# Kernel optimization log

Measured on AMD Instinct MI355X. Metric: run time of the kernel, lower is better.

## Reference

```python
import jax, jax.numpy as jnp
import numpy as np

SEQ_LEN = 1
INPUT = 2048
HIDDEN = 2048
CLASSES = 10
K = int(np.floor(np.sqrt(HIDDEN)))            # avgKernelSize = 45
NUM_EH = (HIDDEN - K) // K + 1                # 45 pooled features
LENGTHS = (32, 128, 512)                      # EHlengths (window sizes)
EST_DIM = NUM_EH * len(LENGTHS) * 2           # mean + variance per (feature, window)
B = 8192


def setup_inputs() -> dict:
    key = jax.random.key(0)
    ks = jax.random.split(key, 7)
    s = 1.0 / np.sqrt(HIDDEN)
    u = lambda k, shape: jax.random.uniform(k, shape, jnp.float32, -s, s)
    return {
        "x": jax.random.normal(ks[0], (B, SEQ_LEN, INPUT), jnp.float32),
        "W_ih": u(ks[1], (HIDDEN, INPUT)),
        "W_hh": u(ks[2], (HIDDEN, HIDDEN)),
        "b_ih": u(ks[3], (HIDDEN,)),
        "b_hh": u(ks[4], (HIDDEN,)),
        "W_lin": u(ks[5], (CLASSES, HIDDEN + EST_DIM)),
        "b_lin": u(ks[6], (CLASSES,)),
    }


def _sliding_stats(pooled):
    """Causal sliding-window mean/variance over the batch/stream axis.

    pooled: (B, F). Returns (B, F, J, 2) with [..., 0]=mean, [..., 1]=var.
    This is the exact quantity the VarEH exponential histograms approximate
    (streaming mean/variance over the last L elements added).
    """
    n = pooled.shape[0]
    cs = jnp.cumsum(pooled, axis=0)
    cs2 = jnp.cumsum(pooled * pooled, axis=0)
    idx = jnp.arange(n)
    outs = []
    for L in LENGTHS:  # small fixed set of window lengths
        zpad = jnp.zeros((L,) + pooled.shape[1:], pooled.dtype)
        cs_l = jnp.concatenate([zpad, cs], axis=0)[:n]
        cs2_l = jnp.concatenate([zpad, cs2], axis=0)[:n]
        cnt = jnp.minimum(idx + 1, L).astype(pooled.dtype)[:, None]
        m = (cs - cs_l) / cnt
        v = (cs2 - cs2_l) / cnt - m * m
        outs.append(jnp.stack([m, v], axis=-1))  # (B, F, 2)
    return jnp.stack(outs, axis=2)  # (B, F, J, 2)


def reference(x, W_ih, W_hh, b_ih, b_hh, W_lin, b_lin):
    b = x.shape[0]
    # Elman RNN, batch_first, h0 = 0. Precompute input projection for all steps.
    xw = jnp.einsum("bsi,hi->bsh", x, W_ih) + b_ih + b_hh  # (B, S, H)

    def step(h, xt):
        h = jnp.tanh(xt + h @ W_hh.T)
        return h, h

    h0 = jnp.zeros((b, HIDDEN), x.dtype)
    _, hs = jax.lax.scan(step, h0, jnp.swapaxes(xw, 0, 1))  # (S, B, H)
    rnn_out = hs[-1]  # (B, H); with seq_len=1 this equals squeeze(rnn_out)

    # AvgPool1d(kernel=K, stride=K) over hidden dim -> (B, NUM_EH)
    pooled = rnn_out[:, : NUM_EH * K].reshape(b, NUM_EH, K).mean(axis=-1)

    # Streaming mean/var estimates across the batch stream (VarEH semantics)
    est = _sliding_stats(pooled).reshape(b, EST_DIM)

    lin_in = jnp.concatenate([rnn_out, est], axis=1)  # (B, H + EST_DIM)
    logits = lin_in @ W_lin.T + b_lin
    return jax.nn.softmax(logits, axis=1)
```

## Files before the change

### kernel.cpp

```cpp
#include <hip/hip_runtime.h>
#include <hip/hip_bf16.h>
#include <math.h>

typedef short s16x8 __attribute__((ext_vector_type(8)));
typedef float f32x4 __attribute__((ext_vector_type(4)));

__device__ inline unsigned short f2bf(float x) {
    unsigned int u = __float_as_uint(x);
    unsigned int r = (u + 0x7fffu + ((u >> 16) & 1u)) >> 16;
    return (unsigned short)r;
}
__device__ inline float bf2f(unsigned short u) {
    return __uint_as_float(((unsigned int)u) << 16);
}

__device__ inline float fast_tanh(float x) {
    float e = __expf(2.0f * x);
    return 1.0f - 2.0f * __builtin_amdgcn_rcpf(e + 1.0f);
}

__global__ void cvtprep_kernel(const float* __restrict__ x,
                               const float* __restrict__ W_ih,
                               const float* __restrict__ W_lin,
                               unsigned short* __restrict__ xb,
                               unsigned short* __restrict__ wb,
                               unsigned short* __restrict__ wlb) {
    int blk = blockIdx.x;
    int tid = threadIdx.x;
    if (blk < 16384) {
        int i = blk * 256 + tid;
        float4 v = ((const float4*)x)[i];
        ushort4 o; o.x = f2bf(v.x); o.y = f2bf(v.y); o.z = f2bf(v.z); o.w = f2bf(v.w);
        ((ushort4*)xb)[i] = o;
    } else if (blk < 20480) {
        int i = (blk - 16384) * 256 + tid;
        float4 v = ((const float4*)W_ih)[i];
        ushort4 o; o.x = f2bf(v.x); o.y = f2bf(v.y); o.z = f2bf(v.z); o.w = f2bf(v.w);
        ((ushort4*)wb)[i] = o;
    } else {
        int idx = (blk - 20480) * 256 + tid;
        if (idx < 37376) {
            int c = idx / 2336, k = idx - c * 2336;
            float v = (c < 10 && k < 2318) ? W_lin[c * 2318 + k] : 0.f;
            wlb[idx] = f2bf(v);
        }
    }
}


#define MFMA_(a, b, c) __builtin_amdgcn_mfma_f32_16x16x32_bf16(a, b, c, 0, 0, 0)

__device__ inline s16x8 frag_ld(const unsigned short* hbase, int row, int ksub, int quad) {
    int slot = (ksub * 4 + quad) ^ (row & 7);
    return *(const s16x8*)(hbase + row * 64 + slot * 8);
}

__device__ inline void stage_u(const unsigned short* __restrict__ gmat, int half,
                               int rowoff, int kt, unsigned short* lmat, int tid) {
    int r = tid >> 3, s = tid & 7;
    int lr = rowoff + r;
    int ks = (s ^ (lr & 7)) << 3;
    const unsigned short* gp = gmat + (size_t)(half * 128 + lr) * 2048 + kt * 64 + ks;
    __builtin_amdgcn_global_load_lds(
        (const __attribute__((address_space(1))) void*)gp,
        (__attribute__((address_space(3))) void*)(lmat + half * 8192 + lr * 64 + s * 8),
        16, 0, 0);
}

#define LOAD_AQ(q)                                                       \
    af0 = frag_ld(Ah, (q) * 32 +      mrow, 0, quad);                    \
    af1 = frag_ld(Ah, (q) * 32 + 16 + mrow, 0, quad);                    \
    af2 = frag_ld(Ah, (q) * 32 +      mrow, 1, quad);                    \
    af3 = frag_ld(Ah, (q) * 32 + 16 + mrow, 1, quad);

#define MFMA_Q(q)                                                        \
    acc[(q)*2 + 0][0] = MFMA_(af0, bf00, acc[(q)*2 + 0][0]);             \
    acc[(q)*2 + 0][1] = MFMA_(af0, bf01, acc[(q)*2 + 0][1]);             \
    acc[(q)*2 + 0][2] = MFMA_(af0, bf02, acc[(q)*2 + 0][2]);             \
    acc[(q)*2 + 0][3] = MFMA_(af0, bf03, acc[(q)*2 + 0][3]);             \
    acc[(q)*2 + 1][0] = MFMA_(af1, bf00, acc[(q)*2 + 1][0]);             \
    acc[(q)*2 + 1][1] = MFMA_(af1, bf01, acc[(q)*2 + 1][1]);             \
    acc[(q)*2 + 1][2] = MFMA_(af1, bf02, acc[(q)*2 + 1][2]);             \
    acc[(q)*2 + 1][3] = MFMA_(af1, bf03, acc[(q)*2 + 1][3]);             \
    acc[(q)*2 + 0][0] = MFMA_(af2, bf10, acc[(q)*2 + 0][0]);             \
    acc[(q)*2 + 0][1] = MFMA_(af2, bf11, acc[(q)*2 + 0][1]);             \
    acc[(q)*2 + 0][2] = MFMA_(af2, bf12, acc[(q)*2 + 0][2]);             \
    acc[(q)*2 + 0][3] = MFMA_(af2, bf13, acc[(q)*2 + 0][3]);             \
    acc[(q)*2 + 1][0] = MFMA_(af3, bf10, acc[(q)*2 + 1][0]);             \
    acc[(q)*2 + 1][1] = MFMA_(af3, bf11, acc[(q)*2 + 1][1]);             \
    acc[(q)*2 + 1][2] = MFMA_(af3, bf12, acc[(q)*2 + 1][2]);             \
    acc[(q)*2 + 1][3] = MFMA_(af3, bf13, acc[(q)*2 + 1][3]);

#define PHASE_CORE(q)                                                    \
    __builtin_amdgcn_s_barrier();                                        \
    asm volatile("s_waitcnt lgkmcnt(0)" ::: "memory");                   \
    __builtin_amdgcn_s_setprio(1);                                       \
    MFMA_Q(q);                                                           \
    __builtin_amdgcn_s_setprio(0);

__global__ __launch_bounds__(512) void gemm_tanh_kernel(
    const unsigned short* __restrict__ A, const unsigned short* __restrict__ Bm,
    const float* __restrict__ b_ih, const float* __restrict__ b_hh,
    unsigned short* __restrict__ Hb)
{
    __shared__ __align__(16) unsigned short lds[2][2][16384];

    const int tid  = threadIdx.x;
    const int lane = tid & 63;
    const int wave = tid >> 6;
    const int wgid = blockIdx.x;
    const int cblk = wgid & 7;
    const int rblk = wgid >> 3;
    const int row0 = rblk * 256;
    const int col0 = cblk * 256;
    const int wm   = wave >> 2;
    const int wn   = wave & 3;
    const int quad = lane >> 4;
    const int mrow = lane & 15;
    const int NT   = 32;

    const unsigned short* Ag = A  + (size_t)row0 * 2048;
    const unsigned short* Bg = Bm + (size_t)col0 * 2048;

    f32x4 acc[8][4];
#pragma unroll
    for (int i = 0; i < 8; ++i)
#pragma unroll
        for (int j = 0; j < 4; ++j) acc[i][j] = f32x4{0.f, 0.f, 0.f, 0.f};

    stage_u(Ag, 0, 0,  0, lds[0][0], tid);  stage_u(Ag, 0, 64, 0, lds[0][0], tid);
    stage_u(Ag, 1, 0,  0, lds[0][0], tid);  stage_u(Ag, 1, 64, 0, lds[0][0], tid);
    stage_u(Bg, 0, 0,  0, lds[0][1], tid);  stage_u(Bg, 0, 64, 0, lds[0][1], tid);
    stage_u(Bg, 1, 0,  0, lds[0][1], tid);  stage_u(Bg, 1, 64, 0, lds[0][1], tid);
    stage_u(Bg, 0, 0,  1, lds[1][1], tid);  stage_u(Bg, 0, 64, 1, lds[1][1], tid);
    stage_u(Bg, 1, 0,  1, lds[1][1], tid);  stage_u(Bg, 1, 64, 1, lds[1][1], tid);
    stage_u(Ag, 0, 0,  1, lds[1][0], tid);  stage_u(Ag, 1, 0,  1, lds[1][0], tid);
    asm volatile("s_waitcnt vmcnt(6)" ::: "memory");
    __builtin_amdgcn_s_barrier();

    for (int t = 0; t < NT; ++t) {
        const int buf = t & 1;
        unsigned short* LA  = lds[buf][0];
        unsigned short* LB  = lds[buf][1];
        unsigned short* NLA = lds[buf ^ 1][0];
        const unsigned short* Ah = LA + wm * 8192;
        const unsigned short* Bh = LB + (wn >> 1) * 8192;
        const int bco = (wn & 1) * 64;

        s16x8 bf00, bf01, bf02, bf03, bf10, bf11, bf12, bf13;
        s16x8 af0, af1, af2, af3;

        bf00 = frag_ld(Bh, bco +  0 + mrow, 0, quad);
        bf01 = frag_ld(Bh, bco + 16 + mrow, 0, quad);
        bf02 = frag_ld(Bh, bco + 32 + mrow, 0, quad);
        bf03 = frag_ld(Bh, bco + 48 + mrow, 0, quad);
        bf10 = frag_ld(Bh, bco +  0 + mrow, 1, quad);
        bf11 = frag_ld(Bh, bco + 16 + mrow, 1, quad);
        bf12 = frag_ld(Bh, bco + 32 + mrow, 1, quad);
        bf13 = frag_ld(Bh, bco + 48 + mrow, 1, quad);
        LOAD_AQ(0);
        if (t + 1 < NT) {
            stage_u(Ag, 0, 64, t + 1, NLA, tid);
            stage_u(Ag, 1, 64, t + 1, NLA, tid);
        }
        asm volatile("s_waitcnt lgkmcnt(8)" ::: "memory");
        PHASE_CORE(0);
        __builtin_amdgcn_s_barrier();

        LOAD_AQ(1);
        if (t + 2 < NT) {
            stage_u(Bg, 0, 0,  t + 2, LB, tid);
            stage_u(Bg, 0, 64, t + 2, LB, tid);
        }
        PHASE_CORE(1);
        __builtin_amdgcn_s_barrier();

        LOAD_AQ(2);
        if (t + 2 < NT) {
            stage_u(Bg, 1, 0,  t + 2, LB, tid);
            stage_u(Bg, 1, 64, t + 2, LB, tid);
        }
        PHASE_CORE(2);
        __builtin_amdgcn_s_barrier();

        LOAD_AQ(3);
        if (t + 2 < NT) {
            stage_u(Ag, 0, 0, t + 2, LA, tid);
            stage_u(Ag, 1, 0, t + 2, LA, tid);
        }
        PHASE_CORE(3);
        if (t + 2 < NT) {
            asm volatile("s_waitcnt vmcnt(6)" ::: "memory");
        } else if (t + 1 < NT) {
            asm volatile("s_waitcnt vmcnt(0)" ::: "memory");
        }
        __builtin_amdgcn_s_barrier();
    }

    float bias[4];
#pragma unroll
    for (int j = 0; j < 4; ++j) {
        int gc = col0 + wn * 64 + j * 16 + mrow;
        bias[j] = b_ih[gc] + b_hh[gc];
    }
#pragma unroll
    for (int i = 0; i < 8; ++i) {
#pragma unroll
        for (int rr = 0; rr < 4; ++rr) {
            int grow = row0 + wm * 128 + i * 16 + quad * 4 + rr;
#pragma unroll
            for (int j = 0; j < 4; ++j) {
                int gc = col0 + wn * 64 + j * 16 + mrow;
                float v = acc[i][j][rr] + bias[j];
                Hb[(size_t)grow * 2048 + gc] = f2bf(fast_tanh(v));
            }
        }
    }
}

__global__ __launch_bounds__(256) void pool_kernel(
    const unsigned short* __restrict__ Hb, float* __restrict__ pooled_t) {
    __shared__ unsigned short hs[8 * 2048];
    __shared__ float outs[45 * 8];
    int b0 = blockIdx.x * 8;
    int tid = threadIdx.x;
    const ushort4* src = (const ushort4*)(Hb + (size_t)b0 * 2048);
    ushort4* dst = (ushort4*)hs;
    for (int i = tid; i < 4096; i += 256) dst[i] = src[i];
    __syncthreads();
    for (int o = tid; o < 360; o += 256) {
        int f = o % 45, r = o / 45;
        const unsigned short* row = hs + r * 2048 + f * 45;
        float s = 0.f;
#pragma unroll
        for (int k = 0; k < 45; ++k) s += bf2f(row[k]);
        outs[f * 8 + r] = s * (1.0f / 45.0f);
    }
    __syncthreads();
    for (int o = tid; o < 360; o += 256) {
        int f = o >> 3, r = o & 7;
        pooled_t[f * 8192 + b0 + r] = outs[o];
    }
}

__global__ __launch_bounds__(256) void scan_kernel(
    const float* __restrict__ pooled_t,
    float* __restrict__ cs_t, float* __restrict__ cs2_t) {
    __shared__ float t1[256], t2[256];
    int f = blockIdx.x;
    int tid = threadIdx.x;
    const float* p = pooled_t + f * 8192;
    int base = tid * 32;
    float loc[32];
    float s1 = 0.f, s2 = 0.f;
#pragma unroll
    for (int i = 0; i < 32; ++i) {
        float v = p[base + i];
        loc[i] = v; s1 += v; s2 += v * v;
    }
    t1[tid] = s1; t2[tid] = s2;
    __syncthreads();
    for (int d = 1; d < 256; d <<= 1) {
        float a1 = (tid >= d) ? t1[tid - d] : 0.f;
        float a2 = (tid >= d) ? t2[tid - d] : 0.f;
        __syncthreads();
        t1[tid] += a1; t2[tid] += a2;
        __syncthreads();
    }
    float r1 = t1[tid] - s1, r2 = t2[tid] - s2;
    float* c1 = cs_t + f * 8192;
    float* c2 = cs2_t + f * 8192;
#pragma unroll
    for (int i = 0; i < 32; ++i) {
        float v = loc[i];
        r1 += v; r2 += v * v;
        c1[base + i] = r1; c2[base + i] = r2;
    }
}

#define ESTRIDE 290
__global__ __launch_bounds__(256) void final_kernel(
    const unsigned short* __restrict__ Hb,
    const float* __restrict__ cs_t, const float* __restrict__ cs2_t,
    const unsigned short* __restrict__ Wb, const float* __restrict__ b_lin,
    float* __restrict__ out) {
    __shared__ unsigned short Es[32 * ESTRIDE];
    __shared__ float comb[2 * 16 * 17];
    int tid = threadIdx.x;
    int lane = tid & 63;
    int wave = tid >> 6;
    int b0 = blockIdx.x * 32;

    for (int i = tid; i < 135 * 32; i += 256) {
        int fj = i >> 5, r = i & 31;
        int f = fj / 3, j = fj - 3 * f;
        int b = b0 + r;
        int L = (j == 0) ? 32 : (j == 1) ? 128 : 512;
        const float* c1 = cs_t + f * 8192;
        const float* c2 = cs2_t + f * 8192;
        float a1 = c1[b], a2 = c2[b];
        float p1 = 0.f, p2 = 0.f;
        if (b >= L) { p1 = c1[b - L]; p2 = c2[b - L]; }
        float cnt = (float)((b + 1 < L) ? (b + 1) : L);
        float m = (a1 - p1) / cnt;
        float v = (a2 - p2) / cnt - m * m;
        int d0 = f * 6 + j * 2;
        Es[r * ESTRIDE + d0]     = f2bf(m);
        Es[r * ESTRIDE + d0 + 1] = f2bf(v);
    }
    for (int i = tid; i < 32 * 18; i += 256) {
        int r = i / 18, d = 270 + i % 18;
        Es[r * ESTRIDE + d] = 0;
    }
    __syncthreads();

    const int t = wave >> 1;
    const int kh = wave & 1;
    const int quad = lane >> 4;
    const int mrow = lane & 15;
    const int rowt = b0 + t * 16;

    f32x4 acc = f32x4{0.f, 0.f, 0.f, 0.f};
    const unsigned short* arow = Hb + (size_t)(rowt + mrow) * 2048 + kh * 1024 + quad * 8;
    const unsigned short* brow = Wb + (size_t)mrow * 2336 + kh * 1024 + quad * 8;
#pragma unroll 4
    for (int k = 0; k < 1024; k += 32) {
        s16x8 a = *(const s16x8*)(arow + k);
        s16x8 b = *(const s16x8*)(brow + k);
        acc = __builtin_amdgcn_mfma_f32_16x16x32_bf16(a, b, acc, 0, 0, 0);
    }
    if (kh) {
        const unsigned short* erow = Es + (t * 16 + mrow) * ESTRIDE + quad * 8;
        const unsigned short* wrow = Wb + (size_t)mrow * 2336 + 2048 + quad * 8;
#pragma unroll
        for (int k = 0; k < 288; k += 32) {
            s16x8 a = *(const s16x8*)(erow + k);
            s16x8 b = *(const s16x8*)(wrow + k);
            acc = __builtin_amdgcn_mfma_f32_16x16x32_bf16(a, b, acc, 0, 0, 0);
        }
    }

    float* cb = comb + t * 272;
    if (kh == 0) {
#pragma unroll
        for (int r = 0; r < 4; ++r) cb[(quad * 4 + r) * 17 + mrow] = acc[r];
    }
    __syncthreads();
    if (kh == 1) {
#pragma unroll
        for (int r = 0; r < 4; ++r) cb[(quad * 4 + r) * 17 + mrow] += acc[r];
    }
    __syncthreads();

    if (tid < 32) {
        const float* base = comb + (tid >> 4) * 272 + (tid & 15) * 17;
        float lg[10];
        float mx = -1e30f;
#pragma unroll
        for (int c = 0; c < 10; ++c) {
            lg[c] = base[c] + b_lin[c];
            mx = fmaxf(mx, lg[c]);
        }
        float s = 0.f;
#pragma unroll
        for (int c = 0; c < 10; ++c) { lg[c] = expf(lg[c] - mx); s += lg[c]; }
        float inv = 1.0f / s;
#pragma unroll
        for (int c = 0; c < 10; ++c) out[(size_t)(b0 + tid) * 10 + c] = lg[c] * inv;
    }
}

extern "C" void kernel_launch(void* const* d_in, const int* in_sizes, int n_in,
                              void* d_out, int out_size, void* d_ws, size_t ws_size,
                              hipStream_t stream) {
    const float* x     = (const float*)d_in[0];
    const float* W_ih  = (const float*)d_in[1];
    const float* b_ih  = (const float*)d_in[3];
    const float* b_hh  = (const float*)d_in[4];
    const float* W_lin = (const float*)d_in[5];
    const float* b_lin = (const float*)d_in[6];
    float* out = (float*)d_out;

    char* ws = (char*)d_ws;
    unsigned short* xb  = (unsigned short*)(ws);
    unsigned short* wb  = (unsigned short*)(ws + 33554432);
    unsigned short* Hb  = (unsigned short*)(ws + 41943040);
    float* pooled_t     = (float*)(ws + 75497472);
    float* cs_t         = (float*)(ws + 76972032);
    float* cs2_t        = (float*)(ws + 78446592);
    unsigned short* wlb = (unsigned short*)(ws + 79921152);

    cvtprep_kernel<<<20626, 256, 0, stream>>>(x, W_ih, W_lin, xb, wb, wlb);
    gemm_tanh_kernel<<<256, 512, 0, stream>>>(xb, wb, b_ih, b_hh, Hb);
    pool_kernel<<<1024, 256, 0, stream>>>(Hb, pooled_t);
    scan_kernel<<<45, 256, 0, stream>>>(pooled_t, cs_t, cs2_t);
    final_kernel<<<256, 256, 0, stream>>>(Hb, cs_t, cs2_t, wlb, b_lin, out);
}
```

Baseline: 224.3 us.

## Restructure GEMM phases to split by k-subtile and remap blocks per XCD

```diff
diff --git a/kernel.cpp b/kernel.cpp
--- a/kernel.cpp
+++ b/kernel.cpp
@@ -67,35 +67,41 @@
         16, 0, 0);
 }
 
-#define LOAD_AQ(q)                                                       \
-    af0 = frag_ld(Ah, (q) * 32 +      mrow, 0, quad);                    \
-    af1 = frag_ld(Ah, (q) * 32 + 16 + mrow, 0, quad);                    \
-    af2 = frag_ld(Ah, (q) * 32 +      mrow, 1, quad);                    \
-    af3 = frag_ld(Ah, (q) * 32 + 16 + mrow, 1, quad);
-
-#define MFMA_Q(q)                                                        \
-    acc[(q)*2 + 0][0] = MFMA_(af0, bf00, acc[(q)*2 + 0][0]);             \
-    acc[(q)*2 + 0][1] = MFMA_(af0, bf01, acc[(q)*2 + 0][1]);             \
-    acc[(q)*2 + 0][2] = MFMA_(af0, bf02, acc[(q)*2 + 0][2]);             \
-    acc[(q)*2 + 0][3] = MFMA_(af0, bf03, acc[(q)*2 + 0][3]);             \
-    acc[(q)*2 + 1][0] = MFMA_(af1, bf00, acc[(q)*2 + 1][0]);             \
-    acc[(q)*2 + 1][1] = MFMA_(af1, bf01, acc[(q)*2 + 1][1]);             \
-    acc[(q)*2 + 1][2] = MFMA_(af1, bf02, acc[(q)*2 + 1][2]);             \
-    acc[(q)*2 + 1][3] = MFMA_(af1, bf03, acc[(q)*2 + 1][3]);             \
-    acc[(q)*2 + 0][0] = MFMA_(af2, bf10, acc[(q)*2 + 0][0]);             \
-    acc[(q)*2 + 0][1] = MFMA_(af2, bf11, acc[(q)*2 + 0][1]);             \
-    acc[(q)*2 + 0][2] = MFMA_(af2, bf12, acc[(q)*2 + 0][2]);             \
-    acc[(q)*2 + 0][3] = MFMA_(af2, bf13, acc[(q)*2 + 0][3]);             \
-    acc[(q)*2 + 1][0] = MFMA_(af3, bf10, acc[(q)*2 + 1][0]);             \
-    acc[(q)*2 + 1][1] = MFMA_(af3, bf11, acc[(q)*2 + 1][1]);             \
-    acc[(q)*2 + 1][2] = MFMA_(af3, bf12, acc[(q)*2 + 1][2]);             \
-    acc[(q)*2 + 1][3] = MFMA_(af3, bf13, acc[(q)*2 + 1][3]);
-
-#define PHASE_CORE(q)                                                    \
+#define LOAD_B(ks)                                                       \
+    b0 = frag_ld(Bh, bco +  0 + mrow, (ks), quad);                       \
+    b1 = frag_ld(Bh, bco + 16 + mrow, (ks), quad);                       \
+    b2 = frag_ld(Bh, bco + 32 + mrow, (ks), quad);                       \
+    b3 = frag_ld(Bh, bco + 48 + mrow, (ks), quad);
+
+#define LOAD_A(h, ks)                                                    \
+    af0 = frag_ld(Ah, (h) * 64 +  0 + mrow, (ks), quad);                 \
+    af1 = frag_ld(Ah, (h) * 64 + 16 + mrow, (ks), quad);                 \
+    af2 = frag_ld(Ah, (h) * 64 + 32 + mrow, (ks), quad);                 \
+    af3 = frag_ld(Ah, (h) * 64 + 48 + mrow, (ks), quad);
+
+#define MFMA_H(hh)                                                       \
+    acc[(hh)*4 + 0][0] = MFMA_(af0, b0, acc[(hh)*4 + 0][0]);             \
+    acc[(hh)*4 + 0][1] = MFMA_(af0, b1, acc[(hh)*4 + 0][1]);             \
+    acc[(hh)*4 + 0][2] = MFMA_(af0, b2, acc[(hh)*4 + 0][2]);             \
+    acc[(hh)*4 + 0][3] = MFMA_(af0, b3, acc[(hh)*4 + 0][3]);             \
+    acc[(hh)*4 + 1][0] = MFMA_(af1, b0, acc[(hh)*4 + 1][0]);             \
+    acc[(hh)*4 + 1][1] = MFMA_(af1, b1, acc[(hh)*4 + 1][1]);             \
+    acc[(hh)*4 + 1][2] = MFMA_(af1, b2, acc[(hh)*4 + 1][2]);             \
+    acc[(hh)*4 + 1][3] = MFMA_(af1, b3, acc[(hh)*4 + 1][3]);             \
+    acc[(hh)*4 + 2][0] = MFMA_(af2, b0, acc[(hh)*4 + 2][0]);             \
+    acc[(hh)*4 + 2][1] = MFMA_(af2, b1, acc[(hh)*4 + 2][1]);             \
+    acc[(hh)*4 + 2][2] = MFMA_(af2, b2, acc[(hh)*4 + 2][2]);             \
+    acc[(hh)*4 + 2][3] = MFMA_(af2, b3, acc[(hh)*4 + 2][3]);             \
+    acc[(hh)*4 + 3][0] = MFMA_(af3, b0, acc[(hh)*4 + 3][0]);             \
+    acc[(hh)*4 + 3][1] = MFMA_(af3, b1, acc[(hh)*4 + 3][1]);             \
+    acc[(hh)*4 + 3][2] = MFMA_(af3, b2, acc[(hh)*4 + 3][2]);             \
+    acc[(hh)*4 + 3][3] = MFMA_(af3, b3, acc[(hh)*4 + 3][3]);
+
+#define PHASE_CORE(hh)                                                   \
     __builtin_amdgcn_s_barrier();                                        \
     asm volatile("s_waitcnt lgkmcnt(0)" ::: "memory");                   \
     __builtin_amdgcn_s_setprio(1);                                       \
-    MFMA_Q(q);                                                           \
+    MFMA_H(hh);                                                          \
     __builtin_amdgcn_s_setprio(0);
 
 __global__ __launch_bounds__(512) void gemm_tanh_kernel(
@@ -109,8 +115,10 @@
     const int lane = tid & 63;
     const int wave = tid >> 6;
     const int wgid = blockIdx.x;
-    const int cblk = wgid & 7;
-    const int rblk = wgid >> 3;
+    const int xcd  = wgid & 7;
+    const int idx  = wgid >> 3;
+    const int rblk = xcd * 4 + (idx & 3);
+    const int cblk = idx >> 2;
     const int row0 = rblk * 256;
     const int col0 = cblk * 256;
     const int wm   = wave >> 2;
@@ -133,9 +141,8 @@
     stage_u(Bg, 0, 0,  0, lds[0][1], tid);  stage_u(Bg, 0, 64, 0, lds[0][1], tid);
     stage_u(Bg, 1, 0,  0, lds[0][1], tid);  stage_u(Bg, 1, 64, 0, lds[0][1], tid);
     stage_u(Bg, 0, 0,  1, lds[1][1], tid);  stage_u(Bg, 0, 64, 1, lds[1][1], tid);
-    stage_u(Bg, 1, 0,  1, lds[1][1], tid);  stage_u(Bg, 1, 64, 1, lds[1][1], tid);
     stage_u(Ag, 0, 0,  1, lds[1][0], tid);  stage_u(Ag, 1, 0,  1, lds[1][0], tid);
-    asm volatile("s_waitcnt vmcnt(6)" ::: "memory");
+    asm volatile("s_waitcnt vmcnt(4)" ::: "memory");
     __builtin_amdgcn_s_barrier();
 
     for (int t = 0; t < NT; ++t) {
@@ -143,54 +150,46 @@
         unsigned short* LA  = lds[buf][0];
         unsigned short* LB  = lds[buf][1];
         unsigned short* NLA = lds[buf ^ 1][0];
+        unsigned short* NLB = lds[buf ^ 1][1];
         const unsigned short* Ah = LA + wm * 8192;
         const unsigned short* Bh = LB + (wn >> 1) * 8192;
         const int bco = (wn & 1) * 64;
 
-        s16x8 bf00, bf01, bf02, bf03, bf10, bf11, bf12, bf13;
+        s16x8 b0, b1, b2, b3;
         s16x8 af0, af1, af2, af3;
 
-        bf00 = frag_ld(Bh, bco +  0 + mrow, 0, quad);
-        bf01 = frag_ld(Bh, bco + 16 + mrow, 0, quad);
-        bf02 = frag_ld(Bh, bco + 32 + mrow, 0, quad);
-        bf03 = frag_ld(Bh, bco + 48 + mrow, 0, quad);
-        bf10 = frag_ld(Bh, bco +  0 + mrow, 1, quad);
-        bf11 = frag_ld(Bh, bco + 16 + mrow, 1, quad);
-        bf12 = frag_ld(Bh, bco + 32 + mrow, 1, quad);
-        bf13 = frag_ld(Bh, bco + 48 + mrow, 1, quad);
-        LOAD_AQ(0);
+        LOAD_B(0);
+        LOAD_A(0, 0);
         if (t + 1 < NT) {
             stage_u(Ag, 0, 64, t + 1, NLA, tid);
             stage_u(Ag, 1, 64, t + 1, NLA, tid);
-        }
-        asm volatile("s_waitcnt lgkmcnt(8)" ::: "memory");
+            stage_u(Bg, 1, 0,  t + 1, NLB, tid);
+            stage_u(Bg, 1, 64, t + 1, NLB, tid);
+        }
+        asm volatile("s_waitcnt lgkmcnt(4)" ::: "memory");
         PHASE_CORE(0);
         __builtin_amdgcn_s_barrier();
 
-        LOAD_AQ(1);
+        LOAD_A(1, 0);
+        PHASE_CORE(1);
+        __builtin_amdgcn_s_barrier();
+
+        LOAD_B(1);
+        LOAD_A(0, 1);
+        asm volatile("s_waitcnt lgkmcnt(4)" ::: "memory");
+        PHASE_CORE(0);
+        __builtin_amdgcn_s_barrier();
+
+        LOAD_A(1, 1);
         if (t + 2 < NT) {
             stage_u(Bg, 0, 0,  t + 2, LB, tid);
             stage_u(Bg, 0, 64, t + 2, LB, tid);
+            stage_u(Ag, 0, 0,  t + 2, LA, tid);
+            stage_u(Ag, 1, 0,  t + 2, LA, tid);
         }
         PHASE_CORE(1);
-        __builtin_amdgcn_s_barrier();
-
-        LOAD_AQ(2);
         if (t + 2 < NT) {
-            stage_u(Bg, 1, 0,  t + 2, LB, tid);
-            stage_u(Bg, 1, 64, t + 2, LB, tid);
-        }
-        PHASE_CORE(2);
-        __builtin_amdgcn_s_barrier();
-
-        LOAD_AQ(3);
-        if (t + 2 < NT) {
-            stage_u(Ag, 0, 0, t + 2, LA, tid);
-            stage_u(Ag, 1, 0, t + 2, LA, tid);
-        }
-        PHASE_CORE(3);
-        if (t + 2 < NT) {
-            asm volatile("s_waitcnt vmcnt(6)" ::: "memory");
+            asm volatile("s_waitcnt vmcnt(4)" ::: "memory");
         } else if (t + 1 < NT) {
             asm volatile("s_waitcnt vmcnt(0)" ::: "memory");
         }
```

Result: no change. 225.1 us (+0.4%).
